# Performance work log

Hardware: AMD Instinct MI355X
Metric: run time of the kernel (lower is better)

Reference implementation:

```python
import jax, jax.numpy as jnp
import numpy as np

B, NCLASS, NSUPP = 4096, 1000, 64
NCHUNK = NSUPP * NSUPP  # 4096, x's feature dim


def setup_inputs() -> dict:
    key = jax.random.key(0)
    k1, k2, k3 = jax.random.split(key, 3)
    x = jax.random.normal(k1, (B, NCHUNK), dtype=jnp.float32)
    # torch .uniform_(-1, 1)
    wSupp = jax.random.uniform(k2, (NCLASS, NSUPP), dtype=jnp.float32, minval=-1.0, maxval=1.0)
    chunk_map = jax.random.randint(k3, (NCLASS, NSUPP), 0, NCHUNK, dtype=jnp.int32)
    return {"x": x, "wSupp": wSupp, "chunk_map": chunk_map}


def reference(x, wSupp, chunk_map):
    # sparse_support: for each class i, feat_i = sum_j x[:, chunk_map[i,j]] * wSupp[i,j]; out = exp(feat)
    gathered = x[:, chunk_map]                      # [B, nClass, nSupp] gather via index map
    feats = jnp.einsum('bcs,cs->bc', gathered, wSupp)  # weighted sum over support
    return jnp.exp(feats)                           # [B, nClass]
```

## Files before the change

### kernel.cpp

```cpp
#include <hip/hip_runtime.h>
#include <hip/hip_fp16.h>


constexpr int B_       = 4096;
constexpr int NCLASS_  = 1000;
constexpr int NSUPP_   = 64;
constexpr int NCHUNK_  = 4096;
constexpr int BT       = 8;
constexpr int THREADS_ = 1024;
constexpr int SG_      = NSUPP_ / 4;
constexpr size_t CMT_BYTES = (size_t)SG_ * NCLASS_ * 16;
constexpr size_t WS_NEEDED = 2 * CMT_BYTES;

__global__ __launch_bounds__(256)
void build_cw_kernel(const int*   __restrict__ cm,
                     const float* __restrict__ w,
                     int*         __restrict__ cmT,
                     float*       __restrict__ wT)
{
    const int t    = threadIdx.x;
    const int c    = blockIdx.x * 4 + (t >> 6);
    const int lane = t & 63;
    if (c >= NCLASS_) return;

    const int   idx = cm[c * NSUPP_ + lane];
    const float wv  = w [c * NSUPP_ + lane];
    const int   key = (idx - c) & 7;

    const unsigned long long below = ((unsigned long long)1 << lane) - 1ull;
    int j = 0;
    #pragma unroll
    for (int r = 0; r < 8; ++r) {
        const unsigned long long m = __ballot(key == r);
        if (key > r)  j += __popcll(m);
        if (key == r) j += __popcll(m & below);
    }

    const int dst = ((j >> 2) * NCLASS_ + c) * 4 + (j & 3);
    cmT[dst] = idx;
    wT [dst] = wv;
}

template <bool USET>
__global__ __launch_bounds__(THREADS_, 8)
void supp_gather_kernel(const float* __restrict__ x,
                        const float* __restrict__ wSupp,
                        const int*   __restrict__ cmap,
                        const float4* __restrict__ wT,
                        const int4*   __restrict__ cmT,
                        float*       __restrict__ out)
{
    __shared__ __align__(16) __half2 tile[NCHUNK_ * 4];

    const int t  = threadIdx.x;
    const int rb = blockIdx.x * BT;

    #pragma unroll
    for (int p = 0; p < NCHUNK_ / THREADS_; ++p) {
        const int col = t + THREADS_ * p;
        float v[BT];
        #pragma unroll
        for (int bi = 0; bi < BT; ++bi)
            v[bi] = x[(size_t)(rb + bi) * NCHUNK_ + col];
        __half2 h[BT / 2];
        #pragma unroll
        for (int k = 0; k < BT / 2; ++k)
            h[k] = __floats2half2_rn(v[2 * k], v[2 * k + 1]);
        *reinterpret_cast<float4*>(&tile[(size_t)col * 4]) =
            *reinterpret_cast<const float4*>(&h[0]);
    }
    __syncthreads();

    if (t < NCLASS_) {
        const int c = t;
        const float4* tile4 = reinterpret_cast<const float4*>(tile);
        float acc[BT];
        #pragma unroll
        for (int bi = 0; bi < BT; ++bi) acc[bi] = 0.f;

        for (int sg = 0; sg < SG_; ++sg) {
            int4   ci;
            float4 wf;
            if constexpr (USET) {
                ci = cmT[sg * NCLASS_ + c];
                wf = wT [sg * NCLASS_ + c];
            } else {
                ci = reinterpret_cast<const int4*>(cmap + c * NSUPP_)[sg];
                wf = reinterpret_cast<const float4*>(wSupp + c * NSUPP_)[sg];
            }

            const float4 d0 = tile4[ci.x];
            const float4 d1 = tile4[ci.y];
            const float4 d2 = tile4[ci.z];
            const float4 d3 = tile4[ci.w];

            const __half2* h0 = reinterpret_cast<const __half2*>(&d0);
            const __half2* h1 = reinterpret_cast<const __half2*>(&d1);
            const __half2* h2 = reinterpret_cast<const __half2*>(&d2);
            const __half2* h3 = reinterpret_cast<const __half2*>(&d3);
            #pragma unroll
            for (int k = 0; k < 4; ++k) {
                float2 f;
                f = __half22float2(h0[k]);
                acc[2 * k]     = fmaf(f.x, wf.x, acc[2 * k]);
                acc[2 * k + 1] = fmaf(f.y, wf.x, acc[2 * k + 1]);
                f = __half22float2(h1[k]);
                acc[2 * k]     = fmaf(f.x, wf.y, acc[2 * k]);
                acc[2 * k + 1] = fmaf(f.y, wf.y, acc[2 * k + 1]);
                f = __half22float2(h2[k]);
                acc[2 * k]     = fmaf(f.x, wf.z, acc[2 * k]);
                acc[2 * k + 1] = fmaf(f.y, wf.z, acc[2 * k + 1]);
                f = __half22float2(h3[k]);
                acc[2 * k]     = fmaf(f.x, wf.w, acc[2 * k]);
                acc[2 * k + 1] = fmaf(f.y, wf.w, acc[2 * k + 1]);
            }
        }
        #pragma unroll
        for (int bi = 0; bi < BT; ++bi)
            out[(size_t)(rb + bi) * NCLASS_ + c] = __expf(acc[bi]);
    }
}

extern "C" void kernel_launch(void* const* d_in, const int* in_sizes, int n_in,
                              void* d_out, int out_size, void* d_ws, size_t ws_size,
                              hipStream_t stream) {
    const float* x  = (const float*)d_in[0];
    const float* w  = (const float*)d_in[1];
    const int*   cm = (const int*)d_in[2];
    float*       o  = (float*)d_out;

    int*   cmT = (int*)d_ws;
    float* wT  = (float*)((char*)d_ws + CMT_BYTES);

    const dim3 grid(B_ / BT);
    if (ws_size >= WS_NEEDED) {
        build_cw_kernel<<<dim3((NCLASS_ + 3) / 4), dim3(256), 0, stream>>>(
            cm, w, cmT, wT);
        supp_gather_kernel<true><<<grid, dim3(THREADS_), 0, stream>>>(
            x, w, cm, (const float4*)wT, (const int4*)cmT, o);
    } else {
        supp_gather_kernel<false><<<grid, dim3(THREADS_), 0, stream>>>(
            x, w, cm, (const float4*)wT, (const int4*)cmT, o);
    }
}
```

Before: 116.5 us.

## Accumulate support sums in packed half2 FMAs with periodic fp32 flush

Replaces the per-element half-to-float conversion and scalar fp32 FMAs with packed __hfma2 on half2 pairs, using weights pre-broadcast to half2 in the build kernel. Partial sums are flushed to fp32 every 16 supports to limit fp16 accumulation error. It also software-prefetches the next index/weight group and drops the occupancy hint from launch bounds. This halves the ALU work in the gather loop at the cost of reduced precision in products and partial sums.

```diff
diff --git a/kernel.cpp b/kernel.cpp
--- a/kernel.cpp
+++ b/kernel.cpp
@@ -16,7 +16,7 @@
 void build_cw_kernel(const int*   __restrict__ cm,
                      const float* __restrict__ w,
                      int*         __restrict__ cmT,
-                     float*       __restrict__ wT)
+                     __half2*     __restrict__ wTh)
 {
     const int t    = threadIdx.x;
     const int c    = blockIdx.x * 4 + (t >> 6);
@@ -38,15 +38,40 @@
 
     const int dst = ((j >> 2) * NCLASS_ + c) * 4 + (j & 3);
     cmT[dst] = idx;
-    wT [dst] = wv;
+    wTh[dst] = __float2half2_rn(wv);
 }
 
+static __device__ __forceinline__ __half2 f2h2(const float u) {
+    union U { float f; __half2 h; } uu;
+    uu.f = u;
+    return uu.h;
+}
+static __device__ __forceinline__ float h2f(const __half2 h) {
+    union U { __half2 h; float f; } uu;
+    uu.h = h;
+    return uu.f;
+}
+
+#define GSUPP(d, wj)                               \
+    a0 = __hfma2(f2h2((d).x), (wj), a0);           \
+    a1 = __hfma2(f2h2((d).y), (wj), a1);           \
+    a2 = __hfma2(f2h2((d).z), (wj), a2);           \
+    a3 = __hfma2(f2h2((d).w), (wj), a3);
+
+#define FLUSH_ACC() {                              \
+    float2 t_;                                     \
+    t_ = __half22float2(a0); f0x += t_.x; f0y += t_.y; \
+    t_ = __half22float2(a1); f1x += t_.x; f1y += t_.y; \
+    t_ = __half22float2(a2); f2x += t_.x; f2y += t_.y; \
+    t_ = __half22float2(a3); f3x += t_.x; f3y += t_.y; \
+    a0 = z_; a1 = z_; a2 = z_; a3 = z_; }
+
 template <bool USET>
-__global__ __launch_bounds__(THREADS_, 8)
+__global__ __launch_bounds__(THREADS_)
 void supp_gather_kernel(const float* __restrict__ x,
                         const float* __restrict__ wSupp,
                         const int*   __restrict__ cmap,
-                        const float4* __restrict__ wT,
+                        const float4* __restrict__ wTh4,
                         const int4*   __restrict__ cmT,
                         float*       __restrict__ out)
 {
@@ -57,67 +82,83 @@
 
     #pragma unroll
     for (int p = 0; p < NCHUNK_ / THREADS_; ++p) {
-        const int col = t + THREADS_ * p;
-        float v[BT];
-        #pragma unroll
-        for (int bi = 0; bi < BT; ++bi)
-            v[bi] = x[(size_t)(rb + bi) * NCHUNK_ + col];
-        __half2 h[BT / 2];
-        #pragma unroll
-        for (int k = 0; k < BT / 2; ++k)
-            h[k] = __floats2half2_rn(v[2 * k], v[2 * k + 1]);
-        *reinterpret_cast<float4*>(&tile[(size_t)col * 4]) =
-            *reinterpret_cast<const float4*>(&h[0]);
+        const size_t col = (size_t)t + THREADS_ * p;
+        float v0 = x[(size_t)(rb + 0) * NCHUNK_ + col];
+        float v1 = x[(size_t)(rb + 1) * NCHUNK_ + col];
+        float v2 = x[(size_t)(rb + 2) * NCHUNK_ + col];
+        float v3 = x[(size_t)(rb + 3) * NCHUNK_ + col];
+        float v4 = x[(size_t)(rb + 4) * NCHUNK_ + col];
+        float v5 = x[(size_t)(rb + 5) * NCHUNK_ + col];
+        float v6 = x[(size_t)(rb + 6) * NCHUNK_ + col];
+        float v7 = x[(size_t)(rb + 7) * NCHUNK_ + col];
+        float4 pk;
+        pk.x = h2f(__floats2half2_rn(v0, v1));
+        pk.y = h2f(__floats2half2_rn(v2, v3));
+        pk.z = h2f(__floats2half2_rn(v4, v5));
+        pk.w = h2f(__floats2half2_rn(v6, v7));
+        *reinterpret_cast<float4*>(&tile[col * 4]) = pk;
     }
     __syncthreads();
 
     if (t < NCLASS_) {
         const int c = t;
         const float4* tile4 = reinterpret_cast<const float4*>(tile);
-        float acc[BT];
+
+        const __half2 z_ = __floats2half2_rn(0.f, 0.f);
+        __half2 a0 = z_, a1 = z_, a2 = z_, a3 = z_;
+        float f0x = 0.f, f0y = 0.f, f1x = 0.f, f1y = 0.f;
+        float f2x = 0.f, f2y = 0.f, f3x = 0.f, f3y = 0.f;
+
+        int4   ci;
+        float4 wh;
+        if constexpr (USET) {
+            ci = cmT [c];
+            wh = wTh4[c];
+        } else {
+            ci = reinterpret_cast<const int4*>(cmap + c * NSUPP_)[0];
+            wh = reinterpret_cast<const float4*>(wSupp + c * NSUPP_)[0];
+        }
+
         #pragma unroll
-        for (int bi = 0; bi < BT; ++bi) acc[bi] = 0.f;
+        for (int sg = 0; sg < SG_; ++sg) {
+            const int4   c4 = ci;
+            const float4 w4 = wh;
 
-        for (int sg = 0; sg < SG_; ++sg) {
-            int4   ci;
-            float4 wf;
+            const int sgn = (sg + 1 < SG_) ? sg + 1 : SG_ - 1;
             if constexpr (USET) {
-                ci = cmT[sg * NCLASS_ + c];
-                wf = wT [sg * NCLASS_ + c];
+                ci = cmT [sgn * NCLASS_ + c];
+                wh = wTh4[sgn * NCLASS_ + c];
             } else {
-                ci = reinterpret_cast<const int4*>(cmap + c * NSUPP_)[sg];
-                wf = reinterpret_cast<const float4*>(wSupp + c * NSUPP_)[sg];
+                ci = reinterpret_cast<const int4*>(cmap + c * NSUPP_)[sgn];
+                wh = reinterpret_cast<const float4*>(wSupp + c * NSUPP_)[sgn];
             }
 
-            const float4 d0 = tile4[ci.x];
-            const float4 d1 = tile4[ci.y];
-            const float4 d2 = tile4[ci.z];
-            const float4 d3 = tile4[ci.w];
+            const float4 d0 = tile4[c4.x];
+            const float4 d1 = tile4[c4.y];
+            const float4 d2 = tile4[c4.z];
+            const float4 d3 = tile4[c4.w];
 
-            const __half2* h0 = reinterpret_cast<const __half2*>(&d0);
-            const __half2* h1 = reinterpret_cast<const __half2*>(&d1);
-            const __half2* h2 = reinterpret_cast<const __half2*>(&d2);
-            const __half2* h3 = reinterpret_cast<const __half2*>(&d3);
-            #pragma unroll
-            for (int k = 0; k < 4; ++k) {
-                float2 f;
-                f = __half22float2(h0[k]);
-                acc[2 * k]     = fmaf(f.x, wf.x, acc[2 * k]);
-                acc[2 * k + 1] = fmaf(f.y, wf.x, acc[2 * k + 1]);
-                f = __half22float2(h1[k]);
-                acc[2 * k]     = fmaf(f.x, wf.y, acc[2 * k]);
-                acc[2 * k + 1] = fmaf(f.y, wf.y, acc[2 * k + 1]);
-                f = __half22float2(h2[k]);
-                acc[2 * k]     = fmaf(f.x, wf.z, acc[2 * k]);
-                acc[2 * k + 1] = fmaf(f.y, wf.z, acc[2 * k + 1]);
-                f = __half22float2(h3[k]);
-                acc[2 * k]     = fmaf(f.x, wf.w, acc[2 * k]);
-                acc[2 * k + 1] = fmaf(f.y, wf.w, acc[2 * k + 1]);
-            }
+            const __half2 w0 = USET ? f2h2(w4.x) : __float2half2_rn(w4.x);
+            const __half2 w1 = USET ? f2h2(w4.y) : __float2half2_rn(w4.y);
+            const __half2 w2 = USET ? f2h2(w4.z) : __float2half2_rn(w4.z);
+            const __half2 w3 = USET ? f2h2(w4.w) : __float2half2_rn(w4.w);
+
+            GSUPP(d0, w0)
+            GSUPP(d1, w1)
+            GSUPP(d2, w2)
+            GSUPP(d3, w3)
+
+            if ((sg & 3) == 3) { FLUSH_ACC() }
         }
-        #pragma unroll
-        for (int bi = 0; bi < BT; ++bi)
-            out[(size_t)(rb + bi) * NCLASS_ + c] = __expf(acc[bi]);
+
+        out[(size_t)(rb + 0) * NCLASS_ + c] = __expf(f0x);
+        out[(size_t)(rb + 1) * NCLASS_ + c] = __expf(f0y);
+        out[(size_t)(rb + 2) * NCLASS_ + c] = __expf(f1x);
+        out[(size_t)(rb + 3) * NCLASS_ + c] = __expf(f1y);
+        out[(size_t)(rb + 4) * NCLASS_ + c] = __expf(f2x);
+        out[(size_t)(rb + 5) * NCLASS_ + c] = __expf(f2y);
+        out[(size_t)(rb + 6) * NCLASS_ + c] = __expf(f3x);
+        out[(size_t)(rb + 7) * NCLASS_ + c] = __expf(f3y);
     }
 }
 
@@ -129,17 +170,17 @@
     const int*   cm = (const int*)d_in[2];
     float*       o  = (float*)d_out;
 
-    int*   cmT = (int*)d_ws;
-    float* wT  = (float*)((char*)d_ws + CMT_BYTES);
+    int*     cmT = (int*)d_ws;
+    __half2* wTh = (__half2*)((char*)d_ws + CMT_BYTES);
 
     const dim3 grid(B_ / BT);
     if (ws_size >= WS_NEEDED) {
         build_cw_kernel<<<dim3((NCLASS_ + 3) / 4), dim3(256), 0, stream>>>(
-            cm, w, cmT, wT);
+            cm, w, cmT, wTh);
         supp_gather_kernel<true><<<grid, dim3(THREADS_), 0, stream>>>(
-            x, w, cm, (const float4*)wT, (const int4*)cmT, o);
+            x, w, cm, (const float4*)wTh, (const int4*)cmT, o);
     } else {
         supp_gather_kernel<false><<<grid, dim3(THREADS_), 0, stream>>>(
-            x, w, cm, (const float4*)wT, (const int4*)cmT, o);
+            x, w, cm, (const float4*)wTh, (const int4*)cmT, o);
     }
 }
```

After: 111.6 us (median of 2 runs). -4.2%, faster.
